# Performance work log

Hardware: AMD Instinct MI355X
Metric: run time of the kernel (lower is better)

## Reference

```python
import jax, jax.numpy as jnp
import numpy as np

B, LS, LH, D1, D2 = 16, 1024, 1024, 1024, 1024


def setup_inputs() -> dict:
    key = jax.random.key(0)
    k1, k2, k3 = jax.random.split(key, 3)
    S = jax.random.normal(k1, (B, LS, D1), dtype=jnp.float32)
    H = jax.random.normal(k2, (B, LH, D2), dtype=jnp.float32)
    pad_mask = jnp.zeros((B, LS, LH), dtype=jnp.float32)  # additive mask
    W_w = jax.random.normal(k3, (D2, D1), dtype=jnp.float32) / np.sqrt(D1)
    W_b = jnp.zeros((D2,), dtype=jnp.float32)
    return {"S": S, "H": H, "pad_mask": pad_mask, "W_w": W_w, "W_b": W_b}


def reference(S, H, pad_mask, W_w, W_b):
    # Linear projection: S_ = S @ W^T + b  -> [B, LS, D2]
    S_ = jnp.einsum('bsd,ed->bse', S, W_w) + W_b
    # Unscaled dot-product scores: [B, LS, LH]
    score = jnp.einsum('bse,bte->bst', S_, H)
    score = score + pad_mask  # additive pad mask
    score = jax.nn.softmax(score, axis=-1)
    # Weighted sum of H: [B, LS, D2]
    out = jnp.einsum('bst,bte->bse', score, H)
    return out
```

## Files before the change

### kernel.cpp

```cpp
#include <hip/hip_runtime.h>
#include <stdint.h>

typedef _Float16 half8 __attribute__((ext_vector_type(8)));
typedef float floatx4 __attribute__((ext_vector_type(4)));

__device__ __forceinline__ uint16_t f16bits(_Float16 h) {
  union { _Float16 f; uint16_t u; } x; x.f = h; return x.u;
}

__device__ __forceinline__ void g2l16(const void* g, void* l) {
  __builtin_amdgcn_global_load_lds((const __attribute__((address_space(1))) void*)g,
                                   (__attribute__((address_space(3))) void*)l,
                                   16, 0, 0);
}

__global__ __launch_bounds__(256) void split_f16_kernel(
    const float* __restrict__ x, uint16_t* __restrict__ hi,
    uint16_t* __restrict__ lo, int n4) {
  int i = blockIdx.x * 256 + threadIdx.x;
  if (i >= n4) return;
  float4 v = ((const float4*)x)[i];
  ushort4 h, l;
  _Float16 a;
  a = (_Float16)v.x; h.x = f16bits(a); l.x = f16bits((_Float16)(v.x - (float)a));
  a = (_Float16)v.y; h.y = f16bits(a); l.y = f16bits((_Float16)(v.y - (float)a));
  a = (_Float16)v.z; h.z = f16bits(a); l.z = f16bits((_Float16)(v.z - (float)a));
  a = (_Float16)v.w; h.w = f16bits(a); l.w = f16bits((_Float16)(v.w - (float)a));
  ((ushort4*)hi)[i] = h;
  ((ushort4*)lo)[i] = l;
}

__global__ __launch_bounds__(256) void split_h_kernel(
    const float* __restrict__ src, uint16_t* __restrict__ hi,
    uint16_t* __restrict__ lo, uint16_t* __restrict__ ht) {
  __shared__ uint16_t tile[64][65];
  const int e0 = blockIdx.x * 64;
  const int t0 = blockIdx.y * 64;
  const size_t bb = (size_t)blockIdx.z << 20;
  const int r = threadIdx.x >> 4;
  const int c = (threadIdx.x & 15) * 4;
#pragma unroll
  for (int it = 0; it < 4; ++it) {
    const int tr = r + it * 16;
    const size_t idx = bb + (size_t)(t0 + tr) * 1024 + e0 + c;
    float4 v = *(const float4*)(src + idx);
    ushort4 h, l;
    _Float16 a;
    a = (_Float16)v.x; h.x = f16bits(a); l.x = f16bits((_Float16)(v.x - (float)a));
    a = (_Float16)v.y; h.y = f16bits(a); l.y = f16bits((_Float16)(v.y - (float)a));
    a = (_Float16)v.z; h.z = f16bits(a); l.z = f16bits((_Float16)(v.z - (float)a));
    a = (_Float16)v.w; h.w = f16bits(a); l.w = f16bits((_Float16)(v.w - (float)a));
    *(ushort4*)(hi + idx) = h;
    *(ushort4*)(lo + idx) = l;
    tile[c + 0][tr] = h.x;
    tile[c + 1][tr] = h.y;
    tile[c + 2][tr] = h.z;
    tile[c + 3][tr] = h.w;
  }
  __syncthreads();
#pragma unroll
  for (int it = 0; it < 4; ++it) {
    const int er = r + it * 16;
    ushort4 o;
    o.x = tile[er][c + 0];
    o.y = tile[er][c + 1];
    o.z = tile[er][c + 2];
    o.w = tile[er][c + 3];
    *(ushort4*)(ht + bb + (size_t)(e0 + er) * 1024 + t0 + c) = o;
  }
}

template <bool SPLIT, int MODE, int GMAP>
__global__ __launch_bounds__(256, 4) void gemm_bt(
    const uint16_t* __restrict__ Ahi, const uint16_t* __restrict__ Alo,
    const uint16_t* __restrict__ Bhi, const uint16_t* __restrict__ Blo,
    uint16_t* __restrict__ Chi, uint16_t* __restrict__ Clo,
    float* __restrict__ Cf, const float* __restrict__ mask,
    const float* __restrict__ bias, int N, int K,
    long batchA, long batchB, long batchC) {
  constexpr int NBUF = SPLIT ? 2 : 1;
  constexpr int LOI = SPLIT ? 1 : 0;
  __shared__ __align__(16) uint16_t sA[2][NBUF][128 * 32];
  __shared__ __align__(16) uint16_t sB[2][NBUF][128 * 32];

  const int tid = threadIdx.x;
  const int lane = tid & 63;
  const int w = tid >> 6;
  const int wr = w >> 1, wc = w & 1;
  const int quad = lane >> 4, l16 = lane & 15;

  int m_t, n_t, z;
  if constexpr (GMAP == 0) {
    m_t = blockIdx.x; n_t = blockIdx.y; z = 0;
  } else {
    z = blockIdx.x; m_t = blockIdx.y >> 3; n_t = blockIdx.y & 7;
  }
  const int m0 = m_t * 128;
  const int n0 = n_t * 128;
  const size_t zA = (size_t)z * batchA;
  const size_t zB = (size_t)z * batchB;
  const size_t zC = (size_t)z * batchC;

  const int r0 = w * 32 + (lane >> 2);
  const int ldc = (((lane & 3) ^ ((lane >> 2) & 3)) * 16);

  const char* gAh0 = (const char*)(Ahi + zA + (size_t)(m0 + r0) * K) + ldc;
  const char* gAh1 = gAh0 + (size_t)16 * K * 2;
  const char* gBh0 = (const char*)(Bhi + zB + (size_t)(n0 + r0) * K) + ldc;
  const char* gBh1 = gBh0 + (size_t)16 * K * 2;
  const char* gAl0 = gAh0; const char* gAl1 = gAh1;
  const char* gBl0 = gBh0; const char* gBl1 = gBh1;
  if constexpr (SPLIT) {
    gAl0 = (const char*)(Alo + zA + (size_t)(m0 + r0) * K) + ldc;
    gAl1 = gAl0 + (size_t)16 * K * 2;
    gBl0 = (const char*)(Blo + zB + (size_t)(n0 + r0) * K) + ldc;
    gBl1 = gBl0 + (size_t)16 * K * 2;
  }

  auto stage = [&](int buf, int kt) {
    const int kb = kt * 64;
    g2l16(gAh0 + kb, &sA[buf][0][(w * 32) * 32]);
    g2l16(gAh1 + kb, &sA[buf][0][(w * 32 + 16) * 32]);
    g2l16(gBh0 + kb, &sB[buf][0][(w * 32) * 32]);
    g2l16(gBh1 + kb, &sB[buf][0][(w * 32 + 16) * 32]);
    if constexpr (SPLIT) {
      g2l16(gAl0 + kb, &sA[buf][LOI][(w * 32) * 32]);
      g2l16(gAl1 + kb, &sA[buf][LOI][(w * 32 + 16) * 32]);
      g2l16(gBl0 + kb, &sB[buf][LOI][(w * 32) * 32]);
      g2l16(gBl1 + kb, &sB[buf][LOI][(w * 32 + 16) * 32]);
    }
  };

  const int aoff = (wr * 64 + l16) * 32 + ((quad ^ (l16 & 3)) * 8);
  const int boff = (wc * 64 + l16) * 32 + ((quad ^ (l16 & 3)) * 8);

  floatx4 acc[4][4];
  floatx4 zero = {0.f, 0.f, 0.f, 0.f};
#pragma unroll
  for (int i = 0; i < 4; ++i)
#pragma unroll
    for (int j = 0; j < 4; ++j) acc[i][j] = zero;

  const int nkt = K >> 5;
  stage(0, 0);
  __syncthreads();
  int cur = 0;
  for (int kt = 0; kt < nkt; ++kt) {
    if (kt + 1 < nkt) stage(cur ^ 1, kt + 1);

    half8 fa[4];
#pragma unroll
    for (int i = 0; i < 4; ++i) fa[i] = *(const half8*)&sA[cur][0][aoff + i * 512];
    if constexpr (SPLIT) {
      half8 fbl[4];
#pragma unroll
      for (int j = 0; j < 4; ++j) fbl[j] = *(const half8*)&sB[cur][1][boff + j * 512];
#pragma unroll
      for (int i = 0; i < 4; ++i)
#pragma unroll
        for (int j = 0; j < 4; ++j)
          acc[i][j] = __builtin_amdgcn_mfma_f32_16x16x32_f16(fa[i], fbl[j], acc[i][j], 0, 0, 0);
    }
    half8 fbh[4];
#pragma unroll
    for (int j = 0; j < 4; ++j) fbh[j] = *(const half8*)&sB[cur][0][boff + j * 512];
#pragma unroll
    for (int i = 0; i < 4; ++i)
#pragma unroll
      for (int j = 0; j < 4; ++j)
        acc[i][j] = __builtin_amdgcn_mfma_f32_16x16x32_f16(fa[i], fbh[j], acc[i][j], 0, 0, 0);
    if constexpr (SPLIT) {
      half8 fal[4];
#pragma unroll
      for (int i = 0; i < 4; ++i) fal[i] = *(const half8*)&sA[cur][1][aoff + i * 512];
#pragma unroll
      for (int i = 0; i < 4; ++i)
#pragma unroll
        for (int j = 0; j < 4; ++j)
          acc[i][j] = __builtin_amdgcn_mfma_f32_16x16x32_f16(fal[i], fbh[j], acc[i][j], 0, 0, 0);
    }
    __syncthreads();
    cur ^= 1;
  }

  const int crow0 = m0 + wr * 64 + quad * 4;
  const int ccol0 = n0 + wc * 64 + l16;
#pragma unroll
  for (int j = 0; j < 4; ++j) {
    const int col = ccol0 + j * 16;
    float bj = 0.f;
    if constexpr (MODE == 0) bj = bias[col];
#pragma unroll
    for (int i = 0; i < 4; ++i) {
#pragma unroll
      for (int r = 0; r < 4; ++r) {
        const int row = crow0 + i * 16 + r;
        const size_t idx = zC + (size_t)row * N + col;
        float v = acc[i][j][r];
        if constexpr (MODE == 0) {
          v += bj;
          _Float16 h = (_Float16)v;
          Chi[idx] = f16bits(h);
          Clo[idx] = f16bits((_Float16)(v - (float)h));
        } else if constexpr (MODE == 1) {
          Cf[idx] = v + mask[idx];
        } else {
          Cf[idx] = v;
        }
      }
    }
  }
}

__global__ __launch_bounds__(256) void softmax_kernel(
    const float* __restrict__ sc, uint16_t* __restrict__ p) {
  const int row = blockIdx.x;
  const float* x = sc + (size_t)row * 1024;
  const int t = threadIdx.x;
  float4 v = ((const float4*)x)[t];
  float m = fmaxf(fmaxf(v.x, v.y), fmaxf(v.z, v.w));
#pragma unroll
  for (int off = 32; off; off >>= 1) m = fmaxf(m, __shfl_xor(m, off));
  __shared__ float redm[4];
  __shared__ float reds[4];
  const int wv = t >> 6, ln = t & 63;
  if (ln == 0) redm[wv] = m;
  __syncthreads();
  m = fmaxf(fmaxf(redm[0], redm[1]), fmaxf(redm[2], redm[3]));
  float e0 = __expf(v.x - m), e1 = __expf(v.y - m);
  float e2 = __expf(v.z - m), e3 = __expf(v.w - m);
  float s = e0 + e1 + e2 + e3;
#pragma unroll
  for (int off = 32; off; off >>= 1) s += __shfl_xor(s, off);
  if (ln == 0) reds[wv] = s;
  __syncthreads();
  s = reds[0] + reds[1] + reds[2] + reds[3];
  float inv = 1.f / s;
  ushort4 o;
  o.x = f16bits((_Float16)(e0 * inv));
  o.y = f16bits((_Float16)(e1 * inv));
  o.z = f16bits((_Float16)(e2 * inv));
  o.w = f16bits((_Float16)(e3 * inv));
  ((ushort4*)(p + (size_t)row * 1024))[t] = o;
}

__global__ __launch_bounds__(256) void transpose_f16_kernel(
    const float* __restrict__ src, uint16_t* __restrict__ dst) {
  __shared__ uint16_t tile[64][65];
  const int e0 = blockIdx.x * 64;
  const int t0 = blockIdx.y * 64;
  const size_t bb = (size_t)blockIdx.z << 20;
  const int r = threadIdx.x >> 4;
  const int c = (threadIdx.x & 15) * 4;
#pragma unroll
  for (int it = 0; it < 4; ++it) {
    const int tr = r + it * 16;
    float4 v = *(const float4*)(src + bb + (size_t)(t0 + tr) * 1024 + e0 + c);
    tile[c + 0][tr] = f16bits((_Float16)v.x);
    tile[c + 1][tr] = f16bits((_Float16)v.y);
    tile[c + 2][tr] = f16bits((_Float16)v.z);
    tile[c + 3][tr] = f16bits((_Float16)v.w);
  }
  __syncthreads();
#pragma unroll
  for (int it = 0; it < 4; ++it) {
    const int er = r + it * 16;
    ushort4 o;
    o.x = tile[er][c + 0];
    o.y = tile[er][c + 1];
    o.z = tile[er][c + 2];
    o.w = tile[er][c + 3];
    *(ushort4*)(dst + bb + (size_t)(e0 + er) * 1024 + t0 + c) = o;
  }
}

extern "C" void kernel_launch(void* const* d_in, const int* in_sizes, int n_in,
                              void* d_out, int out_size, void* d_ws, size_t ws_size,
                              hipStream_t stream) {
  (void)in_sizes; (void)n_in; (void)out_size;
  const float* S    = (const float*)d_in[0];
  const float* H    = (const float*)d_in[1];
  const float* mask = (const float*)d_in[2];
  const float* Ww   = (const float*)d_in[3];
  const float* Wb   = (const float*)d_in[4];
  float* out = (float*)d_out;
  char* ws = (char*)d_ws;
  const size_t MB = 1024ull * 1024ull;

  uint16_t* Whi  = (uint16_t*)(ws + 0 * MB);
  uint16_t* Wlo  = (uint16_t*)(ws + 2 * MB);
  uint16_t* Pjhi = (uint16_t*)(ws + 4 * MB);
  uint16_t* Pjlo = (uint16_t*)(ws + 36 * MB);
  uint16_t* Hhi  = (uint16_t*)(ws + 68 * MB);
  uint16_t* Hlo  = (uint16_t*)(ws + 100 * MB);
  uint16_t* Shi  = (uint16_t*)(ws + 132 * MB);
  uint16_t* Slo  = (uint16_t*)(ws + 164 * MB);
  float*    SC   = (float*)(ws + 132 * MB);
  uint16_t* PR   = (uint16_t*)(ws + 68 * MB);

  const bool roomy = ws_size >= 229ull * MB;
  uint16_t* HT = roomy ? (uint16_t*)(ws + 196 * MB)
                       : (uint16_t*)(ws + 100 * MB);

  split_f16_kernel<<<16384, 256, 0, stream>>>(S, Shi, Slo, 4 * 1024 * 1024);
  split_f16_kernel<<<1024, 256, 0, stream>>>(Ww, Whi, Wlo, 256 * 1024);
  if (roomy) {
    split_h_kernel<<<dim3(16, 16, 16), 256, 0, stream>>>(H, Hhi, Hlo, HT);
  } else {
    split_f16_kernel<<<16384, 256, 0, stream>>>(H, Hhi, Hlo, 4 * 1024 * 1024);
  }

  gemm_bt<true, 0, 0><<<dim3(128, 8, 1), 256, 0, stream>>>(
      Shi, Slo, Whi, Wlo, Pjhi, Pjlo, nullptr, nullptr, Wb,
      1024, 1024, 0, 0, 0);
  gemm_bt<true, 1, 1><<<dim3(16, 64, 1), 256, 0, stream>>>(
      Pjhi, Pjlo, Hhi, Hlo, nullptr, nullptr, SC, mask, nullptr,
      1024, 1024, 1048576, 1048576, 1048576);
  softmax_kernel<<<16384, 256, 0, stream>>>(SC, PR);
  if (!roomy) {
    transpose_f16_kernel<<<dim3(16, 16, 16), 256, 0, stream>>>(H, HT);
  }
  gemm_bt<false, 2, 1><<<dim3(16, 64, 1), 256, 0, stream>>>(
      PR, nullptr, HT, nullptr, nullptr, nullptr, out, nullptr, nullptr,
      1024, 1024, 1048576, 1048576, 1048576);
}
```

Before: 506.3 us.

## Single-buffer B tile in LDS and prefetch only A with explicit vmcnt waits

The B operand tile drops from double to single buffering, which shrinks the LDS footprint of the GEMM kernel, presumably so more workgroups fit per CU. Each iteration now loads its B tile and prefetches the next A tile. Manual s_waitcnt vmcnt counts plus a raw barrier let the kernel wait only for B before the MFMAs. The cost is that B load latency is no longer hidden behind the previous iteration's compute, and there is an extra barrier per k-step.

```diff
diff --git a/kernel.cpp b/kernel.cpp
--- a/kernel.cpp
+++ b/kernel.cpp
@@ -81,7 +81,7 @@
   constexpr int NBUF = SPLIT ? 2 : 1;
   constexpr int LOI = SPLIT ? 1 : 0;
   __shared__ __align__(16) uint16_t sA[2][NBUF][128 * 32];
-  __shared__ __align__(16) uint16_t sB[2][NBUF][128 * 32];
+  __shared__ __align__(16) uint16_t sB[NBUF][128 * 32];
 
   const int tid = threadIdx.x;
   const int lane = tid & 63;
@@ -117,17 +117,22 @@
     gBl1 = gBl0 + (size_t)16 * K * 2;
   }
 
-  auto stage = [&](int buf, int kt) {
+  auto stageA = [&](int buf, int kt) {
     const int kb = kt * 64;
     g2l16(gAh0 + kb, &sA[buf][0][(w * 32) * 32]);
     g2l16(gAh1 + kb, &sA[buf][0][(w * 32 + 16) * 32]);
-    g2l16(gBh0 + kb, &sB[buf][0][(w * 32) * 32]);
-    g2l16(gBh1 + kb, &sB[buf][0][(w * 32 + 16) * 32]);
     if constexpr (SPLIT) {
       g2l16(gAl0 + kb, &sA[buf][LOI][(w * 32) * 32]);
       g2l16(gAl1 + kb, &sA[buf][LOI][(w * 32 + 16) * 32]);
-      g2l16(gBl0 + kb, &sB[buf][LOI][(w * 32) * 32]);
-      g2l16(gBl1 + kb, &sB[buf][LOI][(w * 32 + 16) * 32]);
+    }
+  };
+  auto stageB = [&](int kt) {
+    const int kb = kt * 64;
+    g2l16(gBh0 + kb, &sB[0][(w * 32) * 32]);
+    g2l16(gBh1 + kb, &sB[0][(w * 32 + 16) * 32]);
+    if constexpr (SPLIT) {
+      g2l16(gBl0 + kb, &sB[LOI][(w * 32) * 32]);
+      g2l16(gBl1 + kb, &sB[LOI][(w * 32 + 16) * 32]);
     }
   };
 
@@ -142,19 +147,36 @@
     for (int j = 0; j < 4; ++j) acc[i][j] = zero;
 
   const int nkt = K >> 5;
-  stage(0, 0);
-  __syncthreads();
+  stageA(0, 0);
+  asm volatile("s_waitcnt vmcnt(0)" ::: "memory");
+  __builtin_amdgcn_s_barrier();
+  asm volatile("" ::: "memory");
+
   int cur = 0;
   for (int kt = 0; kt < nkt; ++kt) {
-    if (kt + 1 < nkt) stage(cur ^ 1, kt + 1);
+    stageB(kt);
+    const bool pre = (kt + 1 < nkt);
+    if (pre) stageA(cur ^ 1, kt + 1);
 
     half8 fa[4];
 #pragma unroll
     for (int i = 0; i < 4; ++i) fa[i] = *(const half8*)&sA[cur][0][aoff + i * 512];
+
+    if (pre) {
+      if constexpr (SPLIT)
+        asm volatile("s_waitcnt vmcnt(4)" ::: "memory");
+      else
+        asm volatile("s_waitcnt vmcnt(2)" ::: "memory");
+    } else {
+      asm volatile("s_waitcnt vmcnt(0)" ::: "memory");
+    }
+    __builtin_amdgcn_s_barrier();
+    asm volatile("" ::: "memory");
+
     if constexpr (SPLIT) {
       half8 fbl[4];
 #pragma unroll
-      for (int j = 0; j < 4; ++j) fbl[j] = *(const half8*)&sB[cur][1][boff + j * 512];
+      for (int j = 0; j < 4; ++j) fbl[j] = *(const half8*)&sB[1][boff + j * 512];
 #pragma unroll
       for (int i = 0; i < 4; ++i)
 #pragma unroll
@@ -163,7 +185,7 @@
     }
     half8 fbh[4];
 #pragma unroll
-    for (int j = 0; j < 4; ++j) fbh[j] = *(const half8*)&sB[cur][0][boff + j * 512];
+    for (int j = 0; j < 4; ++j) fbh[j] = *(const half8*)&sB[0][boff + j * 512];
 #pragma unroll
     for (int i = 0; i < 4; ++i)
 #pragma unroll
```

Measured after the change: 499.6 us. No clear change (-1.3%).
